# Optimization experiments

Hardware: AMD Instinct MI355X
Metric: run time of the kernel (lower is better)

Reference implementation:

```python
import jax, jax.numpy as jnp
import numpy as np
from jax import lax

B_J0 = 0.01   # config.b_j0
R_M = 1.0     # config.R_m
BETA = 1.8    # isAdapt=1 branch
GAMMA = 0.5   # config.gamma
LENS = 0.5    # config.lens
SCALE = 6.0   # config.scale
HIGHT = 0.15  # config.hight


def _gauss(x, mu, sigma):
    return jnp.exp(-(x - mu) ** 2 / (2.0 * sigma ** 2)) / jnp.sqrt(2.0 * jnp.pi) / sigma


@jax.custom_vjp
def spike_fn(x):
    return (x > 0).astype(x.dtype)

def _spike_fwd(x):
    return spike_fn(x), x

def _spike_bwd(x, g):
    # 'MG' multi-gaussian surrogate gradient from ActFun_adp.backward
    temp = (_gauss(x, 0.0, LENS) * (1.0 + HIGHT)
            - _gauss(x, LENS, SCALE * LENS) * HIGHT
            - _gauss(x, -LENS, SCALE * LENS) * HIGHT)
    return (g * temp * GAMMA,)

spike_fn.defvjp(_spike_fwd, _spike_bwd)


def setup_inputs() -> dict:
    key = jax.random.key(0)
    ks = jax.random.split(key, 20)
    B, T, I, H, O = 256, 250, 700, 128, 20
    def xav(k, shape):
        lim = jnp.sqrt(6.0 / (shape[0] + shape[1]))
        return jax.random.uniform(k, shape, jnp.float32, -lim, lim)
    def orth(k, n):
        a = jax.random.normal(k, (n, n), jnp.float32)
        q, r = jnp.linalg.qr(a)
        return q * jnp.sign(jnp.diag(r))[None, :]
    return {
        'input': jax.random.normal(ks[0], (B, T, I), jnp.float32),
        'A1_mask': jnp.ones((H, H), jnp.float32),
        'A2_mask': jnp.ones((H, H), jnp.float32),
        'W_ih1': xav(ks[1], (H, I)), 'b_ih1': jnp.zeros((H,), jnp.float32),
        'W_h1h1': orth(ks[2], H), 'b_h1h1': jnp.zeros((H,), jnp.float32),
        'W_h1h2': xav(ks[3], (H, H)), 'b_h1h2': jnp.zeros((H,), jnp.float32),
        'W_h2h2': orth(ks[4], H), 'b_h2h2': jnp.zeros((H,), jnp.float32),
        'W_h2o': xav(ks[5], (O, H)), 'b_h2o': jnp.zeros((O,), jnp.float32),
        'tau_adp_h1': 150.0 + 10.0 * jax.random.normal(ks[6], (H,), jnp.float32),
        'tau_adp_h2': 150.0 + 10.0 * jax.random.normal(ks[7], (H,), jnp.float32),
        'tau_m_h1': 20.0 + 5.0 * jax.random.normal(ks[8], (H,), jnp.float32),
        'tau_m_h2': 20.0 + 5.0 * jax.random.normal(ks[9], (H,), jnp.float32),
        'tau_m_o': 20.0 + 5.0 * jax.random.normal(ks[10], (O,), jnp.float32),
        'hid1_mem0': jax.random.uniform(ks[11], (B, H), jnp.float32),
        'hid2_mem0': jax.random.uniform(ks[12], (B, H), jnp.float32),
        'out_mem0': jax.random.uniform(ks[13], (B, O), jnp.float32),
    }


def reference(input, A1_mask, A2_mask,
              W_ih1, b_ih1, W_h1h1, b_h1h1, W_h1h2, b_h1h2,
              W_h2h2, b_h2h2, W_h2o, b_h2o,
              tau_adp_h1, tau_adp_h2, tau_m_h1, tau_m_h2, tau_m_o,
              hid1_mem0, hid2_mem0, out_mem0):
    B, T, _ = input.shape
    H = W_ih1.shape[0]
    O = W_h2o.shape[0]
    # time-constant decays (dt = 1), computed once
    a1 = jnp.exp(-1.0 / tau_m_h1)
    r1 = jnp.exp(-1.0 / tau_adp_h1)
    a2 = jnp.exp(-1.0 / tau_m_h2)
    r2 = jnp.exp(-1.0 / tau_adp_h2)
    ao = jnp.exp(-1.0 / tau_m_o)

    xT = jnp.swapaxes(input, 0, 1)  # [T, B, I]
    carry0 = (hid1_mem0, jnp.zeros((B, H), input.dtype), jnp.full((B, H), B_J0, input.dtype),
              hid2_mem0, jnp.zeros((B, H), input.dtype), jnp.full((B, H), B_J0, input.dtype),
              out_mem0, jnp.zeros((B, O), input.dtype))

    def step(carry, xs):
        x_t, t = xs
        h1m, h1s, b1, h2m, h2s, b2, om, acc = carry
        # layer 1: input + recurrent drive, adaptive threshold LIF update
        in1 = x_t @ W_ih1.T + b_ih1 + h1s @ W_h1h1.T + b_h1h1
        b1 = r1 * b1 + (1.0 - r1) * h1s
        Bth1 = B_J0 + BETA * b1
        h1m = h1m * a1 + (1.0 - a1) * R_M * in1 - Bth1 * h1s
        h1s = spike_fn(h1m - Bth1)
        # layer 2
        in2 = h1s @ W_h1h2.T + b_h1h2 + h2s @ W_h2h2.T + b_h2h2
        b2 = r2 * b2 + (1.0 - r2) * h2s
        Bth2 = B_J0 + BETA * b2
        h2m = h2m * a2 + (1.0 - a2) * R_M * in2 - Bth2 * h2s
        h2s = spike_fn(h2m - Bth2)
        # leaky-integrator readout (no spike)
        om = om * ao + (1.0 - ao) * R_M * (h2s @ W_h2o.T + b_h2o)
        # accumulate softmax only for t > 10
        acc = acc + jnp.where(t > 10, 1.0, 0.0) * jax.nn.softmax(om, axis=1)
        return (h1m, h1s, b1, h2m, h2s, b2, om, acc), None

    final, _ = lax.scan(step, carry0, (xT, jnp.arange(T)))
    output = final[-1]
    A_norm = jnp.sum(jnp.abs(W_h1h1)) + jnp.sum(jnp.abs(W_h2h2))
    return output, A_norm


if __name__ == '__main__':
    out = reference(**setup_inputs())
    print(out[0].shape, out[1])
```

## Files before the change

### kernel.cpp

```cpp
#include <hip/hip_runtime.h>
#include <hip/hip_bf16.h>
#include <stdint.h>

#define HN 128
#define TSTEPS 250
#define ON 20
#define GK 700
#define NKT 22

typedef _Float16 h2 __attribute__((ext_vector_type(2)));
typedef _Float16 h8 __attribute__((ext_vector_type(8)));
typedef float f4 __attribute__((ext_vector_type(4)));

__device__ __forceinline__ uint32_t pack2u(float x, float y) {
    h2 p; p.x = (_Float16)x; p.y = (_Float16)y;
    return __builtin_bit_cast(uint32_t, p);
}

__global__ __launch_bounds__(256) void ff_gemm(const float* __restrict__ X,
                                               const float* __restrict__ W,
                                               const float* __restrict__ bias,
                                               float* __restrict__ out) {
    __shared__ __align__(16) uint32_t Xs[2][128][16];
    __shared__ __align__(16) uint32_t Ws[2][128][16];
    const int tid   = threadIdx.x;
    const int w     = tid >> 6;
    const int lane  = tid & 63;
    const int m0    = blockIdx.x * 128;
    const int srow  = tid & 127;
    const int shalf = tid >> 7;
    const int lr    = lane & 15;
    const int lg    = lane >> 4;

    f4 acc[2][8];
#pragma unroll
    for (int m = 0; m < 2; ++m)
#pragma unroll
        for (int n = 0; n < 8; ++n) acc[m][n] = (f4){0.f, 0.f, 0.f, 0.f};

    float4 x4[4], w4[4];

#define LOADT(t)                                                               \
    {                                                                          \
        const int k0 = (t) * 32 + shalf * 16;                                  \
        if ((t) < 21 || shalf == 0) {                                          \
            _Pragma("unroll")                                                  \
            for (int q = 0; q < 4; ++q) {                                      \
                x4[q] = *(const float4*)&X[(size_t)(m0 + srow) * GK + k0 + q * 4]; \
                w4[q] = *(const float4*)&W[(size_t)srow * GK + k0 + q * 4];    \
            }                                                                  \
        } else {                                                               \
            _Pragma("unroll")                                                  \
            for (int q = 0; q < 3; ++q) {                                      \
                x4[q] = *(const float4*)&X[(size_t)(m0 + srow) * GK + k0 + q * 4]; \
                w4[q] = *(const float4*)&W[(size_t)srow * GK + k0 + q * 4];    \
            }                                                                  \
            x4[3] = (float4){0.f, 0.f, 0.f, 0.f};                              \
            w4[3] = (float4){0.f, 0.f, 0.f, 0.f};                              \
        }                                                                      \
    }
#define STORET(buf)                                                            \
    {                                                                          \
        _Pragma("unroll")                                                      \
        for (int q = 0; q < 4; ++q) {                                          \
            Xs[buf][srow][shalf * 8 + 2 * q]     = pack2u(x4[q].x, x4[q].y);   \
            Xs[buf][srow][shalf * 8 + 2 * q + 1] = pack2u(x4[q].z, x4[q].w);   \
            Ws[buf][srow][shalf * 8 + 2 * q]     = pack2u(w4[q].x, w4[q].y);   \
            Ws[buf][srow][shalf * 8 + 2 * q + 1] = pack2u(w4[q].z, w4[q].w);   \
        }                                                                      \
    }

    LOADT(0);
    STORET(0);
    __syncthreads();
    int cur = 0;
    for (int t = 0; t < NKT; ++t) {
        if (t + 1 < NKT) LOADT(t + 1);
        h8 a[2];
#pragma unroll
        for (int m = 0; m < 2; ++m) {
            const uint4 au = *(const uint4*)&Xs[cur][w * 32 + m * 16 + lr][lg * 4];
            a[m] = __builtin_bit_cast(h8, au);
        }
#pragma unroll
        for (int n = 0; n < 8; ++n) {
            const uint4 bu = *(const uint4*)&Ws[cur][n * 16 + lr][lg * 4];
            const h8 bf = __builtin_bit_cast(h8, bu);
            acc[0][n] = __builtin_amdgcn_mfma_f32_16x16x32_f16(a[0], bf, acc[0][n], 0, 0, 0);
            acc[1][n] = __builtin_amdgcn_mfma_f32_16x16x32_f16(a[1], bf, acc[1][n], 0, 0, 0);
        }
        if (t + 1 < NKT) STORET(cur ^ 1);
        __syncthreads();
        cur ^= 1;
    }

    float bv[8];
#pragma unroll
    for (int n = 0; n < 8; ++n) bv[n] = bias[n * 16 + lr];
#pragma unroll
    for (int m = 0; m < 2; ++m)
#pragma unroll
        for (int q = 0; q < 4; ++q) {
            const size_t row = (size_t)(m0 + w * 32 + m * 16 + lg * 4 + q);
#pragma unroll
            for (int n = 0; n < 8; ++n)
                out[row * HN + n * 16 + lr] = acc[m][n][q] + bv[n];
        }
#undef LOADT
#undef STORET
}

__device__ __forceinline__ void qrow(const float* __restrict__ src,
                                     uint4 (&wq)[8], float& sc) {
    float amax = 0.f;
#pragma unroll
    for (int q = 0; q < 32; ++q) {
        float4 v = *(const float4*)&src[q * 4];
        amax = fmaxf(amax, fmaxf(fmaxf(fabsf(v.x), fabsf(v.y)),
                                 fmaxf(fabsf(v.z), fabsf(v.w))));
    }
    const float qs = (amax > 0.f) ? 127.f / amax : 0.f;
#pragma unroll
    for (int g = 0; g < 8; ++g) {
        uint32_t u[4];
#pragma unroll
        for (int e = 0; e < 4; ++e) {
            float4 v = *(const float4*)&src[g * 16 + e * 4];
            const int q0 = (int)rintf(v.x * qs), q1 = (int)rintf(v.y * qs);
            const int q2 = (int)rintf(v.z * qs), q3 = (int)rintf(v.w * qs);
            u[e] = (uint32_t)(q0 & 255) | ((uint32_t)(q1 & 255) << 8) |
                   ((uint32_t)(q2 & 255) << 16) | ((uint32_t)(q3 & 255) << 24);
        }
        wq[g].x = u[0]; wq[g].y = u[1]; wq[g].z = u[2]; wq[g].w = u[3];
    }
    sc = (amax > 0.f) ? amax / 127.f : 0.f;
}

__device__ __forceinline__ int mvqr(const uint4 (&wq)[8], const uint4 (&sv)[8]) {
    int a0 = 0, a1 = 0, a2 = 0, a3 = 0;
#pragma unroll
    for (int g = 0; g < 8; ++g) {
        a0 = __builtin_amdgcn_sdot4((int)wq[g].x, (int)sv[g].x, a0, false);
        a1 = __builtin_amdgcn_sdot4((int)wq[g].y, (int)sv[g].y, a1, false);
        a2 = __builtin_amdgcn_sdot4((int)wq[g].z, (int)sv[g].z, a2, false);
        a3 = __builtin_amdgcn_sdot4((int)wq[g].w, (int)sv[g].w, a3, false);
    }
    return (a0 + a1) + (a2 + a3);
}

#define LOADQ(arr, buf, sv)                                                    \
    {                                                                          \
        const uint4* _p = (const uint4*)&arr[buf][0];                          \
        _Pragma("unroll") for (int _g = 0; _g < 8; ++_g) sv[_g] = _p[_g];      \
    }

__device__ __forceinline__ uint32_t nib2bytes(uint32_t nib) {
    return ((nib & 15u) * 0x00204081u) & 0x01010101u;
}

__global__ __launch_bounds__(512) void srnn_pipe11(
    const float* __restrict__ ff,
    const float* __restrict__ W_h1h1, const float* __restrict__ b_h1h1,
    const float* __restrict__ W_h1h2, const float* __restrict__ b_h1h2,
    const float* __restrict__ W_h2h2, const float* __restrict__ b_h2h2,
    const float* __restrict__ W_h2o,  const float* __restrict__ b_h2o,
    const float* __restrict__ tau_adp_h1, const float* __restrict__ tau_adp_h2,
    const float* __restrict__ tau_m_h1,   const float* __restrict__ tau_m_h2,
    const float* __restrict__ tau_m_o,
    const float* __restrict__ h1m0, const float* __restrict__ h2m0,
    const float* __restrict__ om0,
    float* __restrict__ out) {
    const int b    = blockIdx.x;
    const int tid  = threadIdx.x;
    const int w    = tid >> 6;
    const int lane = tid & 63;

    __shared__ __align__(16) uint32_t s1w[2][32];
    __shared__ __align__(16) uint32_t s2w[2][32];
    __shared__ float pBbuf[2][HN];
    __shared__ __align__(16) float rdot_lds[2][32];

    if (tid < 32) {
        s1w[0][tid] = 0u; s1w[1][tid] = 0u;
        s2w[0][tid] = 0u; s2w[1][tid] = 0u;
    }
    __syncthreads();

    if (w < 2) {
        const int j = (w << 6) + lane;
        uint4 wq[8]; float sA;
        qrow(W_h1h1 + j * HN, wq, sA);
        float h1m = h1m0[b * HN + j];
        const float a1 = expf(-1.f / tau_m_h1[j]);
        const float r1 = expf(-1.f / tau_adp_h1[j]);
        const float bi = b_h1h1[j];
        float b1 = 0.01f, s1p = 0.f;
        const float* fp = ff + (size_t)b * TSTEPS * HN + j;
        float fc = fp[0], fn = fp[HN];
        for (int i = 0; i < TSTEPS + 4; ++i) {
            if (i < TSTEPS) {
                const float f2 = (i + 2 < TSTEPS) ? fp[(size_t)(i + 2) * HN] : 0.f;
                uint4 sv[8];
                LOADQ(s1w, (i + 1) & 1, sv);
                const float pA = sA * (float)mvqr(wq, sv);
                b1 = r1 * b1 + (1.f - r1) * s1p;
                const float Bt = 0.01f + 1.8f * b1;
                h1m = h1m * a1 + (1.f - a1) * (fc + bi + pA) - Bt * s1p;
                const int sp = (h1m - Bt > 0.f) ? 1 : 0;
                s1p = (float)sp;
                const unsigned long long mk = __ballot(sp);
                const uint32_t mlo = (uint32_t)mk, mhi = (uint32_t)(mk >> 32);
                if (lane < 16) {
                    const uint32_t nib = (lane < 8 ? mlo : mhi) >> ((lane & 7) * 4);
                    s1w[i & 1][(w << 4) + lane] = nib2bytes(nib);
                }
                fc = fn; fn = f2;
            }
            __syncthreads();
        }
    } else if (w < 4) {
        const int j = ((w - 2) << 6) + lane;
        uint4 wq[8]; float sB;
        qrow(W_h1h2 + j * HN, wq, sB);
        for (int i = 0; i < TSTEPS + 4; ++i) {
            if (i >= 1 && i <= TSTEPS) {
                uint4 sv[8];
                LOADQ(s1w, (i - 1) & 1, sv);
                pBbuf[(i - 1) & 1][j] = sB * (float)mvqr(wq, sv);
            }
            __syncthreads();
        }
    } else if (w < 6) {
        const int j = ((w - 4) << 6) + lane;
        uint4 wq[8]; float sC;
        qrow(W_h2h2 + j * HN, wq, sC);
        float h2m = h2m0[b * HN + j];
        const float a2 = expf(-1.f / tau_m_h2[j]);
        const float r2 = expf(-1.f / tau_adp_h2[j]);
        const float bi = b_h1h2[j] + b_h2h2[j];
        float b2v = 0.01f, s2p = 0.f;
        for (int i = 0; i < TSTEPS + 4; ++i) {
            if (i >= 2 && i <= TSTEPS + 1) {
                const int k2 = i - 2;
                uint4 sv[8];
                LOADQ(s2w, (k2 + 1) & 1, sv);
                const float pC = sC * (float)mvqr(wq, sv);
                const float in2 = pBbuf[k2 & 1][j] + pC + bi;
                b2v = r2 * b2v + (1.f - r2) * s2p;
                const float Bt = 0.01f + 1.8f * b2v;
                h2m = h2m * a2 + (1.f - a2) * in2 - Bt * s2p;
                const int sp = (h2m - Bt > 0.f) ? 1 : 0;
                s2p = (float)sp;
                const unsigned long long mk = __ballot(sp);
                const uint32_t mlo = (uint32_t)mk, mhi = (uint32_t)(mk >> 32);
                if (lane < 16) {
                    const uint32_t nib = (lane < 8 ? mlo : mhi) >> ((lane & 7) * 4);
                    s2w[k2 & 1][((w - 4) << 4) + lane] = nib2bytes(nib);
                }
            }
            __syncthreads();
        }
    } else if (w == 6) {
        const int o = lane;
        uint4 wq[8]; float sO;
        qrow(W_h2o + (size_t)((o < ON) ? o : 0) * HN, wq, sO);
        if (o >= ON) sO = 0.f;
        for (int i = 0; i < TSTEPS + 4; ++i) {
            if (i >= 3 && i <= TSTEPS + 2 && o < ON) {
                const int k3 = i - 3;
                uint4 sv[8];
                LOADQ(s2w, k3 & 1, sv);
                rdot_lds[k3 & 1][o] = sO * (float)mvqr(wq, sv);
            }
            __syncthreads();
        }
    } else {
        float omv[ON], accv[ON], aov[ON], bov[ON];
#pragma unroll
        for (int k = 0; k < ON; ++k) {
            omv[k]  = om0[b * ON + k];
            aov[k]  = expf(-1.f / tau_m_o[k]);
            bov[k]  = b_h2o[k];
            accv[k] = 0.f;
        }
        for (int i = 0; i < TSTEPS + 4; ++i) {
            if (i >= 4) {
                const int k4 = i - 4;
                const float4* rp = (const float4*)&rdot_lds[k4 & 1][0];
                const float4 r0 = rp[0], r1 = rp[1], r2 = rp[2], r3 = rp[3], r4 = rp[4];
                float rd[ON];
                rd[0] = r0.x;  rd[1] = r0.y;  rd[2] = r0.z;  rd[3] = r0.w;
                rd[4] = r1.x;  rd[5] = r1.y;  rd[6] = r1.z;  rd[7] = r1.w;
                rd[8] = r2.x;  rd[9] = r2.y;  rd[10] = r2.z; rd[11] = r2.w;
                rd[12] = r3.x; rd[13] = r3.y; rd[14] = r3.z; rd[15] = r3.w;
                rd[16] = r4.x; rd[17] = r4.y; rd[18] = r4.z; rd[19] = r4.w;
#pragma unroll
                for (int k = 0; k < ON; ++k)
                    omv[k] = omv[k] * aov[k] + (1.f - aov[k]) * (rd[k] + bov[k]);
                float m0 = omv[0], m1 = omv[1], m2 = omv[2], m3 = omv[3];
#pragma unroll
                for (int k = 4; k < ON; k += 4) {
                    m0 = fmaxf(m0, omv[k]);
                    m1 = fmaxf(m1, omv[k + 1]);
                    m2 = fmaxf(m2, omv[k + 2]);
                    m3 = fmaxf(m3, omv[k + 3]);
                }
                const float mx = fmaxf(fmaxf(m0, m1), fmaxf(m2, m3));
                float e[ON];
                float d0 = 0.f, d1 = 0.f, d2 = 0.f, d3 = 0.f;
#pragma unroll
                for (int k = 0; k < ON; k += 4) {
                    e[k]     = __expf(omv[k] - mx);     d0 += e[k];
                    e[k + 1] = __expf(omv[k + 1] - mx); d1 += e[k + 1];
                    e[k + 2] = __expf(omv[k + 2] - mx); d2 += e[k + 2];
                    e[k + 3] = __expf(omv[k + 3] - mx); d3 += e[k + 3];
                }
                const float den = (d0 + d1) + (d2 + d3);
                if (k4 > 10) {
                    const float rden = 1.f / den;
#pragma unroll
                    for (int k = 0; k < ON; ++k)
                        accv[k] = fmaf(e[k], rden, accv[k]);
                }
            }
            __syncthreads();
        }
        if (lane == 0) {
#pragma unroll
            for (int k = 0; k < ON; ++k) out[b * ON + k] = accv[k];
        }
    }
}

__global__ void anorm_kernel(const float* __restrict__ W1,
                             const float* __restrict__ W2,
                             float* __restrict__ out) {
    __shared__ float red[256];
    float s = 0.f;
    for (int i = threadIdx.x; i < HN * HN; i += 256)
        s += fabsf(W1[i]) + fabsf(W2[i]);
    red[threadIdx.x] = s;
    __syncthreads();
    for (int off = 128; off > 0; off >>= 1) {
        if (threadIdx.x < off) red[threadIdx.x] += red[threadIdx.x + off];
        __syncthreads();
    }
    if (threadIdx.x == 0) out[256 * ON] = red[0];
}

extern "C" void kernel_launch(void* const* d_in, const int* in_sizes, int n_in,
                              void* d_out, int out_size, void* d_ws, size_t ws_size,
                              hipStream_t stream) {
    const float* input      = (const float*)d_in[0];
    const float* W_ih1      = (const float*)d_in[3];
    const float* b_ih1      = (const float*)d_in[4];
    const float* W_h1h1     = (const float*)d_in[5];
    const float* b_h1h1     = (const float*)d_in[6];
    const float* W_h1h2     = (const float*)d_in[7];
    const float* b_h1h2     = (const float*)d_in[8];
    const float* W_h2h2     = (const float*)d_in[9];
    const float* b_h2h2     = (const float*)d_in[10];
    const float* W_h2o      = (const float*)d_in[11];
    const float* b_h2o      = (const float*)d_in[12];
    const float* tau_adp_h1 = (const float*)d_in[13];
    const float* tau_adp_h2 = (const float*)d_in[14];
    const float* tau_m_h1   = (const float*)d_in[15];
    const float* tau_m_h2   = (const float*)d_in[16];
    const float* tau_m_o    = (const float*)d_in[17];
    const float* h1m0       = (const float*)d_in[18];
    const float* h2m0       = (const float*)d_in[19];
    const float* om0        = (const float*)d_in[20];

    float* out   = (float*)d_out;
    float* ffbuf = (float*)d_ws;

    anorm_kernel<<<1, 256, 0, stream>>>(W_h1h1, W_h2h2, out);
    ff_gemm<<<500, 256, 0, stream>>>(input, W_ih1, b_ih1, ffbuf);
    srnn_pipe11<<<256, 512, 0, stream>>>(ffbuf, W_h1h1, b_h1h1, W_h1h2, b_h1h2,
                                         W_h2h2, b_h2h2, W_h2o, b_h2o,
                                         tau_adp_h1, tau_adp_h2,
                                         tau_m_h1, tau_m_h2, tau_m_o,
                                         h1m0, h2m0, om0, out);
}
```

Baseline: 224.9 us.

## Replace block barriers with LDS progress-flag ring pipeline across five waves

The recurrent kernel drops its per-step __syncthreads in favour of per-stage progress counters in LDS with 8-deep ring buffers, so each stage waits only on its true producer or consumer. Each wave now handles two neurons per lane, shrinking the block from 8 to 5 waves. The two recurrent layers rebuild their own spike vectors from ballot masks in registers rather than reading them back from LDS. The cost is spin-waiting on volatile LDS and reliance on manual lgkmcnt fences for memory ordering.

```diff
diff --git a/kernel.cpp b/kernel.cpp
--- a/kernel.cpp
+++ b/kernel.cpp
@@ -158,7 +158,29 @@
     return ((nib & 15u) * 0x00204081u) & 0x01010101u;
 }
 
-__global__ __launch_bounds__(512) void srnn_pipe11(
+__device__ __forceinline__ void spread_masks(unsigned long long lo,
+                                             unsigned long long hi,
+                                             uint4 (&sv)[8]) {
+#pragma unroll
+    for (int g = 0; g < 8; ++g) {
+        const unsigned long long src = (g < 4) ? lo : hi;
+        const int base = (g & 3) * 16;
+        sv[g].x = nib2bytes((uint32_t)(src >> (base + 0)));
+        sv[g].y = nib2bytes((uint32_t)(src >> (base + 4)));
+        sv[g].z = nib2bytes((uint32_t)(src >> (base + 8)));
+        sv[g].w = nib2bytes((uint32_t)(src >> (base + 12)));
+    }
+}
+
+#define LDS_FENCE() asm volatile("s_waitcnt lgkmcnt(0)" ::: "memory")
+
+#define PROG_S1 0
+#define PROG_B  1
+#define PROG_C  2
+#define PROG_RO 3
+#define PROG_OM 4
+
+__global__ __launch_bounds__(320) void srnn_pipe12(
     const float* __restrict__ ff,
     const float* __restrict__ W_h1h1, const float* __restrict__ b_h1h1,
     const float* __restrict__ W_h1h2, const float* __restrict__ b_h1h2,
@@ -175,104 +197,139 @@
     const int w    = tid >> 6;
     const int lane = tid & 63;
 
-    __shared__ __align__(16) uint32_t s1w[2][32];
-    __shared__ __align__(16) uint32_t s2w[2][32];
-    __shared__ float pBbuf[2][HN];
-    __shared__ __align__(16) float rdot_lds[2][32];
-
-    if (tid < 32) {
-        s1w[0][tid] = 0u; s1w[1][tid] = 0u;
-        s2w[0][tid] = 0u; s2w[1][tid] = 0u;
-    }
+    __shared__ __align__(16) uint32_t s1ring[8][32];
+    __shared__ __align__(16) uint32_t s2ring[8][32];
+    __shared__ __align__(16) float    pBring[8][HN];
+    __shared__ __align__(16) float    rdring[8][32];
+    __shared__ int prog[8];
+
+    if (tid < 8) prog[tid] = 0;
     __syncthreads();
 
-    if (w < 2) {
-        const int j = (w << 6) + lane;
-        uint4 wq[8]; float sA;
-        qrow(W_h1h1 + j * HN, wq, sA);
-        float h1m = h1m0[b * HN + j];
-        const float a1 = expf(-1.f / tau_m_h1[j]);
-        const float r1 = expf(-1.f / tau_adp_h1[j]);
-        const float bi = b_h1h1[j];
-        float b1 = 0.01f, s1p = 0.f;
-        const float* fp = ff + (size_t)b * TSTEPS * HN + j;
-        float fc = fp[0], fn = fp[HN];
-        for (int i = 0; i < TSTEPS + 4; ++i) {
-            if (i < TSTEPS) {
-                const float f2 = (i + 2 < TSTEPS) ? fp[(size_t)(i + 2) * HN] : 0.f;
-                uint4 sv[8];
-                LOADQ(s1w, (i + 1) & 1, sv);
-                const float pA = sA * (float)mvqr(wq, sv);
-                b1 = r1 * b1 + (1.f - r1) * s1p;
-                const float Bt = 0.01f + 1.8f * b1;
-                h1m = h1m * a1 + (1.f - a1) * (fc + bi + pA) - Bt * s1p;
-                const int sp = (h1m - Bt > 0.f) ? 1 : 0;
-                s1p = (float)sp;
-                const unsigned long long mk = __ballot(sp);
-                const uint32_t mlo = (uint32_t)mk, mhi = (uint32_t)(mk >> 32);
-                if (lane < 16) {
-                    const uint32_t nib = (lane < 8 ? mlo : mhi) >> ((lane & 7) * 4);
-                    s1w[i & 1][(w << 4) + lane] = nib2bytes(nib);
-                }
-                fc = fn; fn = f2;
+#define WAIT_GE(idx, target, cache)                                            \
+    if ((cache) < (target)) {                                                  \
+        volatile int* _p = (volatile int*)&prog[idx];                          \
+        int _v = *_p;                                                          \
+        while (_v < (target)) _v = *_p;                                        \
+        (cache) = _v;                                                          \
+        LDS_FENCE();                                                           \
+    }
+#define PUBLISH(idx, val)                                                      \
+    {                                                                          \
+        LDS_FENCE();                                                           \
+        if (lane == 0) ((volatile int*)prog)[idx] = (val);                     \
+    }
+
+    if (w == 0) {
+        const int jl = lane, jh = lane + 64;
+        uint4 wql[8], wqh[8]; float sAl, sAh;
+        qrow(W_h1h1 + jl * HN, wql, sAl);
+        qrow(W_h1h1 + jh * HN, wqh, sAh);
+        float h1m_l = h1m0[b * HN + jl], h1m_h = h1m0[b * HN + jh];
+        const float a1l = expf(-1.f / tau_m_h1[jl]), a1h = expf(-1.f / tau_m_h1[jh]);
+        const float r1l = expf(-1.f / tau_adp_h1[jl]), r1h = expf(-1.f / tau_adp_h1[jh]);
+        const float bil = b_h1h1[jl], bih = b_h1h1[jh];
+        float b1l = 0.01f, b1h = 0.01f, s1l = 0.f, s1h = 0.f;
+        const float* fpl = ff + (size_t)b * TSTEPS * HN + jl;
+        const float* fph = ff + (size_t)b * TSTEPS * HN + jh;
+        float fcl = fpl[0], fnl = fpl[HN];
+        float fch = fph[0], fnh = fph[HN];
+        unsigned long long mklo = 0ull, mkhi = 0ull;
+        int cB = 0;
+        for (int t = 0; t < TSTEPS; ++t) {
+            const float f2l = (t + 2 < TSTEPS) ? fpl[(size_t)(t + 2) * HN] : 0.f;
+            const float f2h = (t + 2 < TSTEPS) ? fph[(size_t)(t + 2) * HN] : 0.f;
+            uint4 sv[8];
+            spread_masks(mklo, mkhi, sv);
+            const float pAl = sAl * (float)mvqr(wql, sv);
+            const float pAh = sAh * (float)mvqr(wqh, sv);
+            b1l = r1l * b1l + (1.f - r1l) * s1l;
+            b1h = r1h * b1h + (1.f - r1h) * s1h;
+            const float Btl = 0.01f + 1.8f * b1l;
+            const float Bth = 0.01f + 1.8f * b1h;
+            h1m_l = h1m_l * a1l + (1.f - a1l) * (fcl + bil + pAl) - Btl * s1l;
+            h1m_h = h1m_h * a1h + (1.f - a1h) * (fch + bih + pAh) - Bth * s1h;
+            const int spl = (h1m_l - Btl > 0.f) ? 1 : 0;
+            const int sph = (h1m_h - Bth > 0.f) ? 1 : 0;
+            s1l = (float)spl; s1h = (float)sph;
+            mklo = __ballot(spl); mkhi = __ballot(sph);
+            WAIT_GE(PROG_B, t - 7, cB);
+            if (lane < 32) {
+                const unsigned long long src = (lane < 16) ? mklo : mkhi;
+                s1ring[t & 7][lane] = nib2bytes((uint32_t)(src >> ((lane & 15) * 4)));
             }
-            __syncthreads();
-        }
-    } else if (w < 4) {
-        const int j = ((w - 2) << 6) + lane;
-        uint4 wq[8]; float sB;
-        qrow(W_h1h2 + j * HN, wq, sB);
-        for (int i = 0; i < TSTEPS + 4; ++i) {
-            if (i >= 1 && i <= TSTEPS) {
-                uint4 sv[8];
-                LOADQ(s1w, (i - 1) & 1, sv);
-                pBbuf[(i - 1) & 1][j] = sB * (float)mvqr(wq, sv);
+            PUBLISH(PROG_S1, t + 1);
+            fcl = fnl; fnl = f2l; fch = fnh; fnh = f2h;
+        }
+    } else if (w == 1) {
+        const int jl = lane, jh = lane + 64;
+        uint4 wql[8], wqh[8]; float sBl, sBh;
+        qrow(W_h1h2 + jl * HN, wql, sBl);
+        qrow(W_h1h2 + jh * HN, wqh, sBh);
+        int cS1 = 0, cC = 0;
+        for (int t = 0; t < TSTEPS; ++t) {
+            WAIT_GE(PROG_S1, t + 1, cS1);
+            uint4 sv[8];
+            LOADQ(s1ring, t & 7, sv);
+            const float pl = sBl * (float)mvqr(wql, sv);
+            const float ph = sBh * (float)mvqr(wqh, sv);
+            WAIT_GE(PROG_C, t - 7, cC);
+            pBring[t & 7][jl] = pl;
+            pBring[t & 7][jh] = ph;
+            PUBLISH(PROG_B, t + 1);
+        }
+    } else if (w == 2) {
+        const int jl = lane, jh = lane + 64;
+        uint4 wql[8], wqh[8]; float sCl, sCh;
+        qrow(W_h2h2 + jl * HN, wql, sCl);
+        qrow(W_h2h2 + jh * HN, wqh, sCh);
+        float h2m_l = h2m0[b * HN + jl], h2m_h = h2m0[b * HN + jh];
+        const float a2l = expf(-1.f / tau_m_h2[jl]), a2h = expf(-1.f / tau_m_h2[jh]);
+        const float r2l = expf(-1.f / tau_adp_h2[jl]), r2h = expf(-1.f / tau_adp_h2[jh]);
+        const float bil = b_h1h2[jl] + b_h2h2[jl];
+        const float bih = b_h1h2[jh] + b_h2h2[jh];
+        float b2l = 0.01f, b2h = 0.01f, s2l = 0.f, s2h = 0.f;
+        unsigned long long mklo = 0ull, mkhi = 0ull;
+        int cB = 0, cRO = 0;
+        for (int t = 0; t < TSTEPS; ++t) {
+            uint4 sv[8];
+            spread_masks(mklo, mkhi, sv);
+            const float pCl = sCl * (float)mvqr(wql, sv);
+            const float pCh = sCh * (float)mvqr(wqh, sv);
+            WAIT_GE(PROG_B, t + 1, cB);
+            const float pBl = pBring[t & 7][jl];
+            const float pBh = pBring[t & 7][jh];
+            b2l = r2l * b2l + (1.f - r2l) * s2l;
+            b2h = r2h * b2h + (1.f - r2h) * s2h;
+            const float Btl = 0.01f + 1.8f * b2l;
+            const float Bth = 0.01f + 1.8f * b2h;
+            h2m_l = h2m_l * a2l + (1.f - a2l) * (pBl + pCl + bil) - Btl * s2l;
+            h2m_h = h2m_h * a2h + (1.f - a2h) * (pBh + pCh + bih) - Bth * s2h;
+            const int spl = (h2m_l - Btl > 0.f) ? 1 : 0;
+            const int sph = (h2m_h - Bth > 0.f) ? 1 : 0;
+            s2l = (float)spl; s2h = (float)sph;
+            mklo = __ballot(spl); mkhi = __ballot(sph);
+            WAIT_GE(PROG_RO, t - 7, cRO);
+            if (lane < 32) {
+                const unsigned long long src = (lane < 16) ? mklo : mkhi;
+                s2ring[t & 7][lane] = nib2bytes((uint32_t)(src >> ((lane & 15) * 4)));
             }
-            __syncthreads();
-        }
-    } else if (w < 6) {
-        const int j = ((w - 4) << 6) + lane;
-        uint4 wq[8]; float sC;
-        qrow(W_h2h2 + j * HN, wq, sC);
-        float h2m = h2m0[b * HN + j];
-        const float a2 = expf(-1.f / tau_m_h2[j]);
-        const float r2 = expf(-1.f / tau_adp_h2[j]);
-        const float bi = b_h1h2[j] + b_h2h2[j];
-        float b2v = 0.01f, s2p = 0.f;
-        for (int i = 0; i < TSTEPS + 4; ++i) {
-            if (i >= 2 && i <= TSTEPS + 1) {
-                const int k2 = i - 2;
-                uint4 sv[8];
-                LOADQ(s2w, (k2 + 1) & 1, sv);
-                const float pC = sC * (float)mvqr(wq, sv);
-                const float in2 = pBbuf[k2 & 1][j] + pC + bi;
-                b2v = r2 * b2v + (1.f - r2) * s2p;
-                const float Bt = 0.01f + 1.8f * b2v;
-                h2m = h2m * a2 + (1.f - a2) * in2 - Bt * s2p;
-                const int sp = (h2m - Bt > 0.f) ? 1 : 0;
-                s2p = (float)sp;
-                const unsigned long long mk = __ballot(sp);
-                const uint32_t mlo = (uint32_t)mk, mhi = (uint32_t)(mk >> 32);
-                if (lane < 16) {
-                    const uint32_t nib = (lane < 8 ? mlo : mhi) >> ((lane & 7) * 4);
-                    s2w[k2 & 1][((w - 4) << 4) + lane] = nib2bytes(nib);
-                }
-            }
-            __syncthreads();
-        }
-    } else if (w == 6) {
+            PUBLISH(PROG_C, t + 1);
+        }
+    } else if (w == 3) {
         const int o = lane;
         uint4 wq[8]; float sO;
         qrow(W_h2o + (size_t)((o < ON) ? o : 0) * HN, wq, sO);
         if (o >= ON) sO = 0.f;
-        for (int i = 0; i < TSTEPS + 4; ++i) {
-            if (i >= 3 && i <= TSTEPS + 2 && o < ON) {
-                const int k3 = i - 3;
-                uint4 sv[8];
-                LOADQ(s2w, k3 & 1, sv);
-                rdot_lds[k3 & 1][o] = sO * (float)mvqr(wq, sv);
-            }
-            __syncthreads();
+        int cC = 0, cOM = 0;
+        for (int t = 0; t < TSTEPS; ++t) {
+            WAIT_GE(PROG_C, t + 1, cC);
+            uint4 sv[8];
+            LOADQ(s2ring, t & 7, sv);
+            const float r = sO * (float)mvqr(wq, sv);
+            WAIT_GE(PROG_OM, t - 7, cOM);
+            if (o < 32) rdring[t & 7][o] = (o < ON) ? r : 0.f;
+            PUBLISH(PROG_RO, t + 1);
         }
     } else {
         float omv[ON], accv[ON], aov[ON], bov[ON];
@@ -283,53 +340,54 @@
             bov[k]  = b_h2o[k];
             accv[k] = 0.f;
         }
-        for (int i = 0; i < TSTEPS + 4; ++i) {
-            if (i >= 4) {
-                const int k4 = i - 4;
-                const float4* rp = (const float4*)&rdot_lds[k4 & 1][0];
-                const float4 r0 = rp[0], r1 = rp[1], r2 = rp[2], r3 = rp[3], r4 = rp[4];
-                float rd[ON];
-                rd[0] = r0.x;  rd[1] = r0.y;  rd[2] = r0.z;  rd[3] = r0.w;
-                rd[4] = r1.x;  rd[5] = r1.y;  rd[6] = r1.z;  rd[7] = r1.w;
-                rd[8] = r2.x;  rd[9] = r2.y;  rd[10] = r2.z; rd[11] = r2.w;
-                rd[12] = r3.x; rd[13] = r3.y; rd[14] = r3.z; rd[15] = r3.w;
-                rd[16] = r4.x; rd[17] = r4.y; rd[18] = r4.z; rd[19] = r4.w;
+        int cRO = 0;
+        for (int t = 0; t < TSTEPS; ++t) {
+            WAIT_GE(PROG_RO, t + 1, cRO);
+            const float4* rp = (const float4*)&rdring[t & 7][0];
+            const float4 r0 = rp[0], r1 = rp[1], r2 = rp[2], r3 = rp[3], r4 = rp[4];
+            float rd[ON];
+            rd[0] = r0.x;  rd[1] = r0.y;  rd[2] = r0.z;  rd[3] = r0.w;
+            rd[4] = r1.x;  rd[5] = r1.y;  rd[6] = r1.z;  rd[7] = r1.w;
+            rd[8] = r2.x;  rd[9] = r2.y;  rd[10] = r2.z; rd[11] = r2.w;
+            rd[12] = r3.x; rd[13] = r3.y; rd[14] = r3.z; rd[15] = r3.w;
+            rd[16] = r4.x; rd[17] = r4.y; rd[18] = r4.z; rd[19] = r4.w;
+            PUBLISH(PROG_OM, t + 1);
+#pragma unroll
+            for (int k = 0; k < ON; ++k)
+                omv[k] = omv[k] * aov[k] + (1.f - aov[k]) * (rd[k] + bov[k]);
+            float m0 = omv[0], m1 = omv[1], m2 = omv[2], m3 = omv[3];
+#pragma unroll
+            for (int k = 4; k < ON; k += 4) {
+                m0 = fmaxf(m0, omv[k]);
+                m1 = fmaxf(m1, omv[k + 1]);
+                m2 = fmaxf(m2, omv[k + 2]);
+                m3 = fmaxf(m3, omv[k + 3]);
+            }
+            const float mx = fmaxf(fmaxf(m0, m1), fmaxf(m2, m3));
+            float e[ON];
+            float d0 = 0.f, d1 = 0.f, d2 = 0.f, d3 = 0.f;
+#pragma unroll
+            for (int k = 0; k < ON; k += 4) {
+                e[k]     = __expf(omv[k] - mx);     d0 += e[k];
+                e[k + 1] = __expf(omv[k + 1] - mx); d1 += e[k + 1];
+                e[k + 2] = __expf(omv[k + 2] - mx); d2 += e[k + 2];
+                e[k + 3] = __expf(omv[k + 3] - mx); d3 += e[k + 3];
+            }
+            const float den = (d0 + d1) + (d2 + d3);
+            if (t > 10) {
+                const float rden = 1.f / den;
 #pragma unroll
                 for (int k = 0; k < ON; ++k)
-                    omv[k] = omv[k] * aov[k] + (1.f - aov[k]) * (rd[k] + bov[k]);
-                float m0 = omv[0], m1 = omv[1], m2 = omv[2], m3 = omv[3];
-#pragma unroll
-                for (int k = 4; k < ON; k += 4) {
-                    m0 = fmaxf(m0, omv[k]);
-                    m1 = fmaxf(m1, omv[k + 1]);
-                    m2 = fmaxf(m2, omv[k + 2]);
-                    m3 = fmaxf(m3, omv[k + 3]);
-                }
-                const float mx = fmaxf(fmaxf(m0, m1), fmaxf(m2, m3));
-                float e[ON];
-                float d0 = 0.f, d1 = 0.f, d2 = 0.f, d3 = 0.f;
-#pragma unroll
-                for (int k = 0; k < ON; k += 4) {
-                    e[k]     = __expf(omv[k] - mx);     d0 += e[k];
-                    e[k + 1] = __expf(omv[k + 1] - mx); d1 += e[k + 1];
-                    e[k + 2] = __expf(omv[k + 2] - mx); d2 += e[k + 2];
-                    e[k + 3] = __expf(omv[k + 3] - mx); d3 += e[k + 3];
-                }
-                const float den = (d0 + d1) + (d2 + d3);
-                if (k4 > 10) {
-                    const float rden = 1.f / den;
-#pragma unroll
-                    for (int k = 0; k < ON; ++k)
-                        accv[k] = fmaf(e[k], rden, accv[k]);
-                }
+                    accv[k] = fmaf(e[k], rden, accv[k]);
             }
-            __syncthreads();
         }
         if (lane == 0) {
 #pragma unroll
             for (int k = 0; k < ON; ++k) out[b * ON + k] = accv[k];
         }
     }
+#undef WAIT_GE
+#undef PUBLISH
 }
 
 __global__ void anorm_kernel(const float* __restrict__ W1,
@@ -376,7 +434,7 @@
 
     anorm_kernel<<<1, 256, 0, stream>>>(W_h1h1, W_h2h2, out);
     ff_gemm<<<500, 256, 0, stream>>>(input, W_ih1, b_ih1, ffbuf);
-    srnn_pipe11<<<256, 512, 0, stream>>>(ffbuf, W_h1h1, b_h1h1, W_h1h2, b_h1h2,
+    srnn_pipe12<<<256, 320, 0, stream>>>(ffbuf, W_h1h1, b_h1h1, W_h1h2, b_h1h2,
                                          W_h2h2, b_h2h2, W_h2o, b_h2o,
                                          tau_adp_h1, tau_adp_h2,
                                          tau_m_h1, tau_m_h2, tau_m_o,
```

New measurement: 239.2 us. 6.3% more time.
